# Kernel tuning notes

Hardware: AMD Instinct MI355X
Metric: run time of the kernel (lower is better)

Reference implementation:

```python
import jax, jax.numpy as jnp
import numpy as np

N = 100000
E = 1600000
IN_CH = 128
EDGE_CH = 16
HID = 128
OUT = 4
EPS = 1e-12  # F.normalize eps


def l2_normalize(x):
    # matches torch.nn.functional.normalize(x, p=2, dim=1)
    norm = jnp.sqrt(jnp.sum(x * x, axis=1, keepdims=True))
    return x / jnp.maximum(norm, EPS)


def sage_conv(x, row, col, edge_attr, W, b, n_nodes):
    # gather source node feats, concat edge feats: [E, in+edge]
    m = jnp.concatenate([x[row], edge_attr], axis=1)
    m = l2_normalize(m)
    # scatter-mean by destination node
    s = jax.ops.segment_sum(m, col, num_segments=n_nodes)
    cnt = jax.ops.segment_sum(jnp.ones((m.shape[0],), m.dtype), col, num_segments=n_nodes)
    agg = s / jnp.maximum(cnt, 1.0)[:, None]
    out = agg @ W + b
    return l2_normalize(out)


def setup_inputs() -> dict:
    key = jax.random.key(0)
    ks = jax.random.split(key, 7)
    x = jax.random.normal(ks[0], (N, IN_CH), dtype=jnp.float32)
    edge_index = jax.random.randint(ks[1], (2, E), 0, N, dtype=jnp.int64)
    edge_attr = jax.random.normal(ks[2], (E, EDGE_CH), dtype=jnp.float32)
    W1 = jax.random.normal(ks[3], (IN_CH + EDGE_CH, HID), dtype=jnp.float32) / np.sqrt(IN_CH + EDGE_CH)
    b1 = jnp.zeros((HID,), dtype=jnp.float32)
    W2 = jax.random.normal(ks[4], (HID + EDGE_CH, OUT), dtype=jnp.float32) / np.sqrt(HID + EDGE_CH)
    b2 = jnp.zeros((OUT,), dtype=jnp.float32)
    return {"x": x, "edge_index": edge_index, "edge_attr": edge_attr,
            "W1": W1, "b1": b1, "W2": W2, "b2": b2}


def reference(x, edge_index, edge_attr, W1, b1, W2, b2):
    row, col = edge_index[0], edge_index[1]
    h = sage_conv(x, row, col, edge_attr, W1, b1, N)
    h = jax.nn.relu(h)  # dropout is identity in eval mode
    h = sage_conv(h, row, col, edge_attr, W2, b2, N)
    return jax.nn.sigmoid(h)
```

## Files before the change

### kernel.cpp

```cpp
#include <hip/hip_runtime.h>
#include <hip/hip_fp16.h>
#include <math.h>

#define N_NODES 100000
#define N_EDGES 1600000
#define CHUNK 1024
#define NCHUNKS ((N_NODES + CHUNK - 1) / CHUNK)

union H8 { uint4 u; __half2 h[4]; };

__device__ __forceinline__ float red32(float v) {
    #pragma unroll
    for (int m = 16; m >= 1; m >>= 1) v += __shfl_xor(v, m, 64);
    return v;
}

__global__ __launch_bounds__(256) void hist(const int* __restrict__ col,
                                            int* __restrict__ cnt) {
    int e = blockIdx.x * blockDim.x + threadIdx.x;
    if (e >= N_EDGES) return;
    atomicAdd(&cnt[col[e]], 1);
}

__global__ void scan_part(const int* __restrict__ cnt, int* __restrict__ psum) {
    __shared__ int sd[CHUNK];
    int i = blockIdx.x * CHUNK + threadIdx.x;
    sd[threadIdx.x] = (i < N_NODES) ? cnt[i] : 0;
    __syncthreads();
    for (int s = CHUNK / 2; s > 0; s >>= 1) {
        if (threadIdx.x < s) sd[threadIdx.x] += sd[threadIdx.x + s];
        __syncthreads();
    }
    if (threadIdx.x == 0) psum[blockIdx.x] = sd[0];
}

__global__ void scan_top(const int* __restrict__ psum, int* __restrict__ coff,
                         int* __restrict__ off) {
    if (blockIdx.x == 0 && threadIdx.x == 0) {
        int run = 0;
        for (int i = 0; i < NCHUNKS; ++i) { coff[i] = run; run += psum[i]; }
        off[N_NODES] = N_EDGES;
    }
}

__global__ void scan_apply(const int* __restrict__ cnt, const int* __restrict__ coff,
                           int* __restrict__ off, int* __restrict__ head) {
    __shared__ int sd[CHUNK];
    int i = blockIdx.x * CHUNK + threadIdx.x;
    int v = (i < N_NODES) ? cnt[i] : 0;
    sd[threadIdx.x] = v;
    __syncthreads();
    for (int s = 1; s < CHUNK; s <<= 1) {
        int t = (threadIdx.x >= s) ? sd[threadIdx.x - s] : 0;
        __syncthreads();
        sd[threadIdx.x] += t;
        __syncthreads();
    }
    if (i < N_NODES) {
        int excl = coff[blockIdx.x] + sd[threadIdx.x] - v;
        off[i] = excl;
        head[i] = excl;
    }
}

__global__ __launch_bounds__(256) void gemm_y1h(const float* __restrict__ x,
                                                const float* __restrict__ W1,
                                                __half* __restrict__ y1h,
                                                float* __restrict__ nx) {
    __shared__ float xs[64][129];
    int r0 = blockIdx.x * 64;
    int t = threadIdx.x;
    for (int i = t; i < 64 * 32; i += 256) {
        int rr = i >> 5, c4 = (i & 31) * 4;
        int gr = r0 + rr;
        float4 v = (gr < N_NODES) ? *(const float4*)(x + (size_t)gr * 128 + c4)
                                  : make_float4(0.f, 0.f, 0.f, 0.f);
        xs[rr][c4] = v.x; xs[rr][c4 + 1] = v.y; xs[rr][c4 + 2] = v.z; xs[rr][c4 + 3] = v.w;
    }
    __syncthreads();
    {
        int rr = t >> 2, q = t & 3;
        float s = 0.f;
        #pragma unroll
        for (int k = 0; k < 32; ++k) { float v = xs[rr][q * 32 + k]; s += v * v; }
        s += __shfl_xor(s, 1, 64);
        s += __shfl_xor(s, 2, 64);
        if (q == 0 && r0 + rr < N_NODES) nx[r0 + rr] = s;
    }
    int tx = t & 31, ty = t >> 5;
    float4 acc[8];
    #pragma unroll
    for (int i = 0; i < 8; ++i) acc[i] = make_float4(0.f, 0.f, 0.f, 0.f);
    #pragma unroll 4
    for (int k = 0; k < 128; ++k) {
        float4 wv = *(const float4*)(W1 + (size_t)k * 128 + tx * 4);
        #pragma unroll
        for (int i = 0; i < 8; ++i) {
            float xv = xs[ty * 8 + i][k];
            acc[i].x += xv * wv.x; acc[i].y += xv * wv.y;
            acc[i].z += xv * wv.z; acc[i].w += xv * wv.w;
        }
    }
    #pragma unroll
    for (int i = 0; i < 8; ++i) {
        int rr = r0 + ty * 8 + i;
        if (rr < N_NODES) {
            H8 pk;
            pk.h[0] = __float22half2_rn(make_float2(acc[i].x, acc[i].y));
            pk.h[1] = __float22half2_rn(make_float2(acc[i].z, acc[i].w));
            *(uint2*)(y1h + (size_t)rr * 128 + tx * 4) = make_uint2(pk.u.x, pk.u.y);
        }
    }
}

__global__ __launch_bounds__(256) void scatter_e(
        const int* __restrict__ row, const int* __restrict__ col,
        const float* __restrict__ nx, const float* __restrict__ ea,
        int* __restrict__ head, int4* __restrict__ csrM) {
    int e = blockIdx.x * blockDim.x + threadIdx.x;
    if (e >= N_EDGES) return;
    const float4* p = (const float4*)(ea + (size_t)e * 16);
    float4 q0 = p[0], q1 = p[1], q2 = p[2], q3 = p[3];
    float s = q0.x*q0.x + q0.y*q0.y + q0.z*q0.z + q0.w*q0.w
            + q1.x*q1.x + q1.y*q1.y + q1.z*q1.z + q1.w*q1.w
            + q2.x*q2.x + q2.y*q2.y + q2.z*q2.z + q2.w*q2.w
            + q3.x*q3.x + q3.y*q3.y + q3.z*q3.z + q3.w*q3.w;
    int r = row[e];
    int c = col[e];
    float w1 = rsqrtf(fmaxf(nx[r] + s, 1e-24f));
    int pp = atomicAdd(&head[c], 1);
    int4 mt; mt.x = r; mt.y = __float_as_int(w1); mt.z = e; mt.w = __float_as_int(s);
    csrM[pp] = mt;
}

__global__ __launch_bounds__(256) void layer1(
        const __half* __restrict__ y1h, const float* __restrict__ ea,
        const int4* __restrict__ csrM, const int* __restrict__ off,
        const float* __restrict__ W1, const float* __restrict__ b1,
        const float* __restrict__ W2,
        float* __restrict__ hn, float4* __restrict__ peaC) {
    __shared__ int4  smeta[4][64];
    __shared__ float strans[4][144];
    int wv = threadIdx.x >> 6;
    int node = (blockIdx.x << 2) | wv;
    int lane = threadIdx.x & 63;
    if (node >= N_NODES) return;
    int s = off[node], e = off[node + 1];
    int deg = e - s;
    int m = (deg < 64) ? deg : 64;
    if (lane < m) smeta[wv][lane] = csrM[s + lane];
    asm volatile("s_waitcnt lgkmcnt(0)" ::: "memory");

    int e4 = lane >> 4;
    int c8 = lane & 15;
    int wrow = (c8 & 3) * 4;
    float4 w2r0 = *(const float4*)(W2 + (size_t)(128 + wrow + 0) * 4);
    float4 w2r1 = *(const float4*)(W2 + (size_t)(128 + wrow + 1) * 4);
    float4 w2r2 = *(const float4*)(W2 + (size_t)(128 + wrow + 2) * 4);
    float4 w2r3 = *(const float4*)(W2 + (size_t)(128 + wrow + 3) * 4);

    float4 a0 = make_float4(0,0,0,0), a1 = a0;
    float4 sea = a0;

    for (int t = 0; t < m; t += 4) {
        int idx = t + e4;
        bool val = idx < m;
        int4 mt = smeta[wv][val ? idx : 0];
        int r = mt.x;
        float w = val ? __int_as_float(mt.y) : 0.f;
        H8 pk; pk.u = *(const uint4*)(y1h + (size_t)r * 128 + c8 * 8);
        float2 f0 = __half22float2(pk.h[0]);
        float2 f1 = __half22float2(pk.h[1]);
        float2 f2 = __half22float2(pk.h[2]);
        float2 f3 = __half22float2(pk.h[3]);
        a0.x += f0.x * w; a0.y += f0.y * w; a0.z += f1.x * w; a0.w += f1.y * w;
        a1.x += f2.x * w; a1.y += f2.y * w; a1.z += f3.x * w; a1.w += f3.y * w;
        if (c8 < 4) {
            float4 ev = *(const float4*)(ea + (size_t)mt.z * 16 + c8 * 4);
            sea.x += ev.x * w; sea.y += ev.y * w;
            sea.z += ev.z * w; sea.w += ev.w * w;
            float4 pv;
            pv.x = ev.x*w2r0.x + ev.y*w2r1.x + ev.z*w2r2.x + ev.w*w2r3.x;
            pv.y = ev.x*w2r0.y + ev.y*w2r1.y + ev.z*w2r2.y + ev.w*w2r3.y;
            pv.z = ev.x*w2r0.z + ev.y*w2r1.z + ev.z*w2r2.z + ev.w*w2r3.z;
            pv.w = ev.x*w2r0.w + ev.y*w2r1.w + ev.z*w2r2.w + ev.w*w2r3.w;
            pv.x += __shfl_xor(pv.x, 1, 64); pv.y += __shfl_xor(pv.y, 1, 64);
            pv.z += __shfl_xor(pv.z, 1, 64); pv.w += __shfl_xor(pv.w, 1, 64);
            pv.x += __shfl_xor(pv.x, 2, 64); pv.y += __shfl_xor(pv.y, 2, 64);
            pv.z += __shfl_xor(pv.z, 2, 64); pv.w += __shfl_xor(pv.w, 2, 64);
            if (c8 == 0 && val) peaC[s + idx] = pv;
        }
    }
    for (int t = 64 + e4; t < deg; t += 4) {
        int4 mt = csrM[s + t];
        int r = mt.x;
        float w = __int_as_float(mt.y);
        H8 pk; pk.u = *(const uint4*)(y1h + (size_t)r * 128 + c8 * 8);
        float2 f0 = __half22float2(pk.h[0]);
        float2 f1 = __half22float2(pk.h[1]);
        float2 f2 = __half22float2(pk.h[2]);
        float2 f3 = __half22float2(pk.h[3]);
        a0.x += f0.x * w; a0.y += f0.y * w; a0.z += f1.x * w; a0.w += f1.y * w;
        a1.x += f2.x * w; a1.y += f2.y * w; a1.z += f3.x * w; a1.w += f3.y * w;
        if (c8 < 4) {
            float4 ev = *(const float4*)(ea + (size_t)mt.z * 16 + c8 * 4);
            sea.x += ev.x * w; sea.y += ev.y * w;
            sea.z += ev.z * w; sea.w += ev.w * w;
            float4 pv;
            pv.x = ev.x*w2r0.x + ev.y*w2r1.x + ev.z*w2r2.x + ev.w*w2r3.x;
            pv.y = ev.x*w2r0.y + ev.y*w2r1.y + ev.z*w2r2.y + ev.w*w2r3.y;
            pv.z = ev.x*w2r0.z + ev.y*w2r1.z + ev.z*w2r2.z + ev.w*w2r3.z;
            pv.w = ev.x*w2r0.w + ev.y*w2r1.w + ev.z*w2r2.w + ev.w*w2r3.w;
            pv.x += __shfl_xor(pv.x, 1, 64); pv.y += __shfl_xor(pv.y, 1, 64);
            pv.z += __shfl_xor(pv.z, 1, 64); pv.w += __shfl_xor(pv.w, 1, 64);
            pv.x += __shfl_xor(pv.x, 2, 64); pv.y += __shfl_xor(pv.y, 2, 64);
            pv.z += __shfl_xor(pv.z, 2, 64); pv.w += __shfl_xor(pv.w, 2, 64);
            if (c8 == 0) peaC[s + t] = pv;
        }
    }
    #pragma unroll
    for (int mm = 16; mm <= 32; mm <<= 1) {
        a0.x += __shfl_xor(a0.x, mm, 64); a0.y += __shfl_xor(a0.y, mm, 64);
        a0.z += __shfl_xor(a0.z, mm, 64); a0.w += __shfl_xor(a0.w, mm, 64);
        a1.x += __shfl_xor(a1.x, mm, 64); a1.y += __shfl_xor(a1.y, mm, 64);
        a1.z += __shfl_xor(a1.z, mm, 64); a1.w += __shfl_xor(a1.w, mm, 64);
        sea.x += __shfl_xor(sea.x, mm, 64); sea.y += __shfl_xor(sea.y, mm, 64);
        sea.z += __shfl_xor(sea.z, mm, 64); sea.w += __shfl_xor(sea.w, mm, 64);
    }
    if (e4 == 0) {
        *(float4*)&strans[wv][c8 * 8]     = a0;
        *(float4*)&strans[wv][c8 * 8 + 4] = a1;
        if (c8 < 4) *(float4*)&strans[wv][128 + c8 * 4] = sea;
    }
    asm volatile("s_waitcnt lgkmcnt(0)" ::: "memory");

    int c = lane & 31;
    float ic = 1.0f / fmaxf((float)deg, 1.0f);
    float4 av = *(const float4*)&strans[wv][c * 4];
    float4 b1v = *(const float4*)(b1 + c * 4);
    float4 o;
    o.x = av.x * ic + b1v.x; o.y = av.y * ic + b1v.y;
    o.z = av.z * ic + b1v.z; o.w = av.w * ic + b1v.w;
    #pragma unroll
    for (int k = 0; k < 16; ++k) {
        float sk = strans[wv][128 + k] * ic;
        float4 wv4 = *((const float4*)(W1 + (size_t)(128 + k) * 128) + c);
        o.x += sk * wv4.x; o.y += sk * wv4.y; o.z += sk * wv4.z; o.w += sk * wv4.w;
    }
    float ss    = o.x*o.x + o.y*o.y + o.z*o.z + o.w*o.w;
    float sspos = (o.x > 0.f ? o.x*o.x : 0.f) + (o.y > 0.f ? o.y*o.y : 0.f)
                + (o.z > 0.f ? o.z*o.z : 0.f) + (o.w > 0.f ? o.w*o.w : 0.f);
    ss = red32(ss);
    sspos = red32(sspos);
    float inv = rsqrtf(fmaxf(ss, 1e-24f));
    float4 h4;
    h4.x = fmaxf(o.x * inv, 0.f); h4.y = fmaxf(o.y * inv, 0.f);
    h4.z = fmaxf(o.z * inv, 0.f); h4.w = fmaxf(o.w * inv, 0.f);
    float nhv = sspos * inv * inv;
    float4 w0 = *(const float4*)(W2 + (size_t)(4*c + 0) * 4);
    float4 w1 = *(const float4*)(W2 + (size_t)(4*c + 1) * 4);
    float4 w2 = *(const float4*)(W2 + (size_t)(4*c + 2) * 4);
    float4 w3 = *(const float4*)(W2 + (size_t)(4*c + 3) * 4);
    float4 p;
    p.x = h4.x*w0.x + h4.y*w1.x + h4.z*w2.x + h4.w*w3.x;
    p.y = h4.x*w0.y + h4.y*w1.y + h4.z*w2.y + h4.w*w3.y;
    p.z = h4.x*w0.z + h4.y*w1.z + h4.z*w2.z + h4.w*w3.z;
    p.w = h4.x*w0.w + h4.y*w1.w + h4.z*w2.w + h4.w*w3.w;
    p.x = red32(p.x); p.y = red32(p.y); p.z = red32(p.z); p.w = red32(p.w);
    if (lane == 0) {
        *(float4*)(hn + (size_t)node * 8) = p;
        hn[(size_t)node * 8 + 4] = nhv;
    }
}

__global__ __launch_bounds__(256) void layer2(
        const int4* __restrict__ csrM, const float4* __restrict__ peaC,
        const float* __restrict__ hn, const int* __restrict__ off,
        const float* __restrict__ b2, float* __restrict__ out) {
    int wv = threadIdx.x >> 6;
    int node = (blockIdx.x << 2) | wv;
    int lane = threadIdx.x & 63;
    if (node >= N_NODES) return;
    int s = off[node], e = off[node + 1];
    int deg = e - s;
    float4 acc = make_float4(0.f, 0.f, 0.f, 0.f);
    for (int t = lane; t < deg; t += 64) {
        int4 mt = csrM[s + t];
        int r = mt.x;
        float sq = __int_as_float(mt.w);
        float4 yh = *(const float4*)(hn + (size_t)r * 8);
        float nh = hn[(size_t)r * 8 + 4];
        float w = rsqrtf(fmaxf(nh + sq, 1e-24f));
        float4 pe = peaC[s + t];
        acc.x += (yh.x + pe.x) * w; acc.y += (yh.y + pe.y) * w;
        acc.z += (yh.z + pe.z) * w; acc.w += (yh.w + pe.w) * w;
    }
    #pragma unroll
    for (int mm = 32; mm >= 1; mm >>= 1) {
        acc.x += __shfl_xor(acc.x, mm, 64);
        acc.y += __shfl_xor(acc.y, mm, 64);
        acc.z += __shfl_xor(acc.z, mm, 64);
        acc.w += __shfl_xor(acc.w, mm, 64);
    }
    if (lane == 0) {
        float ic = 1.0f / fmaxf((float)deg, 1.0f);
        float4 o;
        o.x = acc.x * ic + b2[0]; o.y = acc.y * ic + b2[1];
        o.z = acc.z * ic + b2[2]; o.w = acc.w * ic + b2[3];
        float ss = o.x*o.x + o.y*o.y + o.z*o.z + o.w*o.w;
        float inv = rsqrtf(fmaxf(ss, 1e-24f));
        float4 res;
        res.x = 1.0f / (1.0f + expf(-(o.x * inv)));
        res.y = 1.0f / (1.0f + expf(-(o.y * inv)));
        res.z = 1.0f / (1.0f + expf(-(o.z * inv)));
        res.w = 1.0f / (1.0f + expf(-(o.w * inv)));
        *(float4*)(out + (size_t)node * 4) = res;
    }
}

extern "C" void kernel_launch(void* const* d_in, const int* in_sizes, int n_in,
                              void* d_out, int out_size, void* d_ws, size_t ws_size,
                              hipStream_t stream) {
    const float* x   = (const float*)d_in[0];
    const int*   ei  = (const int*)d_in[1];
    const float* ea  = (const float*)d_in[2];
    const float* W1  = (const float*)d_in[3];
    const float* b1  = (const float*)d_in[4];
    const float* W2  = (const float*)d_in[5];
    const float* b2  = (const float*)d_in[6];
    const int* row = ei;
    const int* col = ei + N_EDGES;
    float* out = (float*)d_out;

    char* ws = (char*)d_ws;
    size_t o = 0;
    auto carve = [&](size_t bytes) { char* p = ws + o; o = (o + bytes + 255) & ~(size_t)255; return p; };
    __half* y1h    = (__half*)carve((size_t)N_NODES * 128 * 2);
    int4*   csrM   = (int4*)carve((size_t)N_EDGES * 16);
    float4* peaC   = (float4*)carve((size_t)N_EDGES * 16);
    int*    cnt    = (int*)carve((size_t)N_NODES * 4);
    int*    off    = (int*)carve((size_t)(N_NODES + 1) * 4);
    int*    head   = (int*)carve((size_t)N_NODES * 4);
    float*  nx     = (float*)carve((size_t)N_NODES * 4);
    float*  hn     = (float*)carve((size_t)N_NODES * 8 * 4);
    int*    psum   = (int*)carve((size_t)NCHUNKS * 4);
    int*    coff   = (int*)carve((size_t)NCHUNKS * 4);
    (void)ws_size; (void)in_sizes; (void)n_in; (void)out_size;

    hipMemsetAsync(cnt, 0, (size_t)N_NODES * 4, stream);

    dim3 b256(256);
    hist<<<(N_EDGES + 255) / 256, b256, 0, stream>>>(col, cnt);
    gemm_y1h<<<(N_NODES + 63) / 64, b256, 0, stream>>>(x, W1, y1h, nx);

    scan_part<<<NCHUNKS, CHUNK, 0, stream>>>(cnt, psum);
    scan_top<<<1, 64, 0, stream>>>(psum, coff, off);
    scan_apply<<<NCHUNKS, CHUNK, 0, stream>>>(cnt, coff, off, head);
    scatter_e<<<(N_EDGES + 255) / 256, b256, 0, stream>>>(row, col, nx, ea, head, csrM);

    layer1<<<(N_NODES + 3) / 4, b256, 0, stream>>>(y1h, ea, csrM, off, W1, b1, W2,
                                                   hn, peaC);
    layer2<<<(N_NODES + 3) / 4, b256, 0, stream>>>(csrM, peaC, hn, off, b2, out);
}
```

Baseline: 408.6 us.

## Drop per-edge projected edge-attr buffer; aggregate edge attrs in layer2 then project

Layer1 no longer computes and stores a per-edge projection of edge attributes through W2 (peaC, 25.6 MB written and read back). Layer2 instead re-reads the raw edge attributes, accumulates them weighted per node, and projects the aggregate once through W2. This also restructures layer2 to cache edge metadata in shared memory and use 16 edges x 4 lanes per wave. It trades a write plus read of peaC for a 64-byte gather of edge_attr per edge in layer2, and adds an unroll hint to layer1's main loop.

```diff
diff --git a/kernel.cpp b/kernel.cpp
--- a/kernel.cpp
+++ b/kernel.cpp
@@ -137,8 +137,7 @@
         const __half* __restrict__ y1h, const float* __restrict__ ea,
         const int4* __restrict__ csrM, const int* __restrict__ off,
         const float* __restrict__ W1, const float* __restrict__ b1,
-        const float* __restrict__ W2,
-        float* __restrict__ hn, float4* __restrict__ peaC) {
+        const float* __restrict__ W2, float* __restrict__ hn) {
     __shared__ int4  smeta[4][64];
     __shared__ float strans[4][144];
     int wv = threadIdx.x >> 6;
@@ -153,15 +152,10 @@
 
     int e4 = lane >> 4;
     int c8 = lane & 15;
-    int wrow = (c8 & 3) * 4;
-    float4 w2r0 = *(const float4*)(W2 + (size_t)(128 + wrow + 0) * 4);
-    float4 w2r1 = *(const float4*)(W2 + (size_t)(128 + wrow + 1) * 4);
-    float4 w2r2 = *(const float4*)(W2 + (size_t)(128 + wrow + 2) * 4);
-    float4 w2r3 = *(const float4*)(W2 + (size_t)(128 + wrow + 3) * 4);
-
     float4 a0 = make_float4(0,0,0,0), a1 = a0;
     float4 sea = a0;
 
+    #pragma unroll 2
     for (int t = 0; t < m; t += 4) {
         int idx = t + e4;
         bool val = idx < m;
@@ -179,16 +173,6 @@
             float4 ev = *(const float4*)(ea + (size_t)mt.z * 16 + c8 * 4);
             sea.x += ev.x * w; sea.y += ev.y * w;
             sea.z += ev.z * w; sea.w += ev.w * w;
-            float4 pv;
-            pv.x = ev.x*w2r0.x + ev.y*w2r1.x + ev.z*w2r2.x + ev.w*w2r3.x;
-            pv.y = ev.x*w2r0.y + ev.y*w2r1.y + ev.z*w2r2.y + ev.w*w2r3.y;
-            pv.z = ev.x*w2r0.z + ev.y*w2r1.z + ev.z*w2r2.z + ev.w*w2r3.z;
-            pv.w = ev.x*w2r0.w + ev.y*w2r1.w + ev.z*w2r2.w + ev.w*w2r3.w;
-            pv.x += __shfl_xor(pv.x, 1, 64); pv.y += __shfl_xor(pv.y, 1, 64);
-            pv.z += __shfl_xor(pv.z, 1, 64); pv.w += __shfl_xor(pv.w, 1, 64);
-            pv.x += __shfl_xor(pv.x, 2, 64); pv.y += __shfl_xor(pv.y, 2, 64);
-            pv.z += __shfl_xor(pv.z, 2, 64); pv.w += __shfl_xor(pv.w, 2, 64);
-            if (c8 == 0 && val) peaC[s + idx] = pv;
         }
     }
     for (int t = 64 + e4; t < deg; t += 4) {
@@ -206,16 +190,6 @@
             float4 ev = *(const float4*)(ea + (size_t)mt.z * 16 + c8 * 4);
             sea.x += ev.x * w; sea.y += ev.y * w;
             sea.z += ev.z * w; sea.w += ev.w * w;
-            float4 pv;
-            pv.x = ev.x*w2r0.x + ev.y*w2r1.x + ev.z*w2r2.x + ev.w*w2r3.x;
-            pv.y = ev.x*w2r0.y + ev.y*w2r1.y + ev.z*w2r2.y + ev.w*w2r3.y;
-            pv.z = ev.x*w2r0.z + ev.y*w2r1.z + ev.z*w2r2.z + ev.w*w2r3.z;
-            pv.w = ev.x*w2r0.w + ev.y*w2r1.w + ev.z*w2r2.w + ev.w*w2r3.w;
-            pv.x += __shfl_xor(pv.x, 1, 64); pv.y += __shfl_xor(pv.y, 1, 64);
-            pv.z += __shfl_xor(pv.z, 1, 64); pv.w += __shfl_xor(pv.w, 1, 64);
-            pv.x += __shfl_xor(pv.x, 2, 64); pv.y += __shfl_xor(pv.y, 2, 64);
-            pv.z += __shfl_xor(pv.z, 2, 64); pv.w += __shfl_xor(pv.w, 2, 64);
-            if (c8 == 0) peaC[s + t] = pv;
         }
     }
     #pragma unroll
@@ -274,39 +248,74 @@
 }
 
 __global__ __launch_bounds__(256) void layer2(
-        const int4* __restrict__ csrM, const float4* __restrict__ peaC,
+        const int4* __restrict__ csrM, const float* __restrict__ ea,
         const float* __restrict__ hn, const int* __restrict__ off,
-        const float* __restrict__ b2, float* __restrict__ out) {
+        const float* __restrict__ W2, const float* __restrict__ b2,
+        float* __restrict__ out) {
+    __shared__ int4 smeta[4][64];
     int wv = threadIdx.x >> 6;
     int node = (blockIdx.x << 2) | wv;
     int lane = threadIdx.x & 63;
     if (node >= N_NODES) return;
     int s = off[node], e = off[node + 1];
     int deg = e - s;
+    int m = (deg < 64) ? deg : 64;
+    if (lane < m) smeta[wv][lane] = csrM[s + lane];
+    asm volatile("s_waitcnt lgkmcnt(0)" ::: "memory");
+    int e16 = lane >> 2, q = lane & 3;
+    float4 w2r0 = *(const float4*)(W2 + (size_t)(128 + q * 4 + 0) * 4);
+    float4 w2r1 = *(const float4*)(W2 + (size_t)(128 + q * 4 + 1) * 4);
+    float4 w2r2 = *(const float4*)(W2 + (size_t)(128 + q * 4 + 2) * 4);
+    float4 w2r3 = *(const float4*)(W2 + (size_t)(128 + q * 4 + 3) * 4);
+
     float4 acc = make_float4(0.f, 0.f, 0.f, 0.f);
-    for (int t = lane; t < deg; t += 64) {
+    float4 sea = make_float4(0.f, 0.f, 0.f, 0.f);
+    for (int t = e16; t < m; t += 16) {
+        int4 mt = smeta[wv][t];
+        int r = mt.x;
+        float sq = __int_as_float(mt.w);
+        float nh = hn[(size_t)r * 8 + 4];
+        float w = rsqrtf(fmaxf(nh + sq, 1e-24f));
+        float4 yh = *(const float4*)(hn + (size_t)r * 8);
+        float4 ev = *(const float4*)(ea + (size_t)mt.z * 16 + q * 4);
+        acc.x += w * yh.x; acc.y += w * yh.y; acc.z += w * yh.z; acc.w += w * yh.w;
+        sea.x += w * ev.x; sea.y += w * ev.y; sea.z += w * ev.z; sea.w += w * ev.w;
+    }
+    for (int t = 64 + e16; t < deg; t += 16) {
         int4 mt = csrM[s + t];
         int r = mt.x;
         float sq = __int_as_float(mt.w);
-        float4 yh = *(const float4*)(hn + (size_t)r * 8);
         float nh = hn[(size_t)r * 8 + 4];
         float w = rsqrtf(fmaxf(nh + sq, 1e-24f));
-        float4 pe = peaC[s + t];
-        acc.x += (yh.x + pe.x) * w; acc.y += (yh.y + pe.y) * w;
-        acc.z += (yh.z + pe.z) * w; acc.w += (yh.w + pe.w) * w;
-    }
-    #pragma unroll
-    for (int mm = 32; mm >= 1; mm >>= 1) {
-        acc.x += __shfl_xor(acc.x, mm, 64);
-        acc.y += __shfl_xor(acc.y, mm, 64);
-        acc.z += __shfl_xor(acc.z, mm, 64);
-        acc.w += __shfl_xor(acc.w, mm, 64);
+        float4 yh = *(const float4*)(hn + (size_t)r * 8);
+        float4 ev = *(const float4*)(ea + (size_t)mt.z * 16 + q * 4);
+        acc.x += w * yh.x; acc.y += w * yh.y; acc.z += w * yh.z; acc.w += w * yh.w;
+        sea.x += w * ev.x; sea.y += w * ev.y; sea.z += w * ev.z; sea.w += w * ev.w;
+    }
+    #pragma unroll
+    for (int mm = 4; mm <= 32; mm <<= 1) {
+        acc.x += __shfl_xor(acc.x, mm, 64); acc.y += __shfl_xor(acc.y, mm, 64);
+        acc.z += __shfl_xor(acc.z, mm, 64); acc.w += __shfl_xor(acc.w, mm, 64);
+        sea.x += __shfl_xor(sea.x, mm, 64); sea.y += __shfl_xor(sea.y, mm, 64);
+        sea.z += __shfl_xor(sea.z, mm, 64); sea.w += __shfl_xor(sea.w, mm, 64);
+    }
+    float4 pv;
+    pv.x = sea.x*w2r0.x + sea.y*w2r1.x + sea.z*w2r2.x + sea.w*w2r3.x;
+    pv.y = sea.x*w2r0.y + sea.y*w2r1.y + sea.z*w2r2.y + sea.w*w2r3.y;
+    pv.z = sea.x*w2r0.z + sea.y*w2r1.z + sea.z*w2r2.z + sea.w*w2r3.z;
+    pv.w = sea.x*w2r0.w + sea.y*w2r1.w + sea.z*w2r2.w + sea.w*w2r3.w;
+    #pragma unroll
+    for (int mm = 1; mm <= 2; mm <<= 1) {
+        pv.x += __shfl_xor(pv.x, mm, 64); pv.y += __shfl_xor(pv.y, mm, 64);
+        pv.z += __shfl_xor(pv.z, mm, 64); pv.w += __shfl_xor(pv.w, mm, 64);
     }
     if (lane == 0) {
         float ic = 1.0f / fmaxf((float)deg, 1.0f);
         float4 o;
-        o.x = acc.x * ic + b2[0]; o.y = acc.y * ic + b2[1];
-        o.z = acc.z * ic + b2[2]; o.w = acc.w * ic + b2[3];
+        o.x = (acc.x + pv.x) * ic + b2[0];
+        o.y = (acc.y + pv.y) * ic + b2[1];
+        o.z = (acc.z + pv.z) * ic + b2[2];
+        o.w = (acc.w + pv.w) * ic + b2[3];
         float ss = o.x*o.x + o.y*o.y + o.z*o.z + o.w*o.w;
         float inv = rsqrtf(fmaxf(ss, 1e-24f));
         float4 res;
@@ -337,7 +346,6 @@
     auto carve = [&](size_t bytes) { char* p = ws + o; o = (o + bytes + 255) & ~(size_t)255; return p; };
     __half* y1h    = (__half*)carve((size_t)N_NODES * 128 * 2);
     int4*   csrM   = (int4*)carve((size_t)N_EDGES * 16);
-    float4* peaC   = (float4*)carve((size_t)N_EDGES * 16);
     int*    cnt    = (int*)carve((size_t)N_NODES * 4);
     int*    off    = (int*)carve((size_t)(N_NODES + 1) * 4);
     int*    head   = (int*)carve((size_t)N_NODES * 4);
@@ -358,7 +366,6 @@
     scan_apply<<<NCHUNKS, CHUNK, 0, stream>>>(cnt, coff, off, head);
     scatter_e<<<(N_EDGES + 255) / 256, b256, 0, stream>>>(row, col, nx, ea, head, csrM);
 
-    layer1<<<(N_NODES + 3) / 4, b256, 0, stream>>>(y1h, ea, csrM, off, W1, b1, W2,
-                                                   hn, peaC);
-    layer2<<<(N_NODES + 3) / 4, b256, 0, stream>>>(csrM, peaC, hn, off, b2, out);
-}
+    layer1<<<(N_NODES + 3) / 4, b256, 0, stream>>>(y1h, ea, csrM, off, W1, b1, W2, hn);
+    layer2<<<(N_NODES + 3) / 4, b256, 0, stream>>>(csrM, ea, hn, off, W2, b2, out);
+}
```

Result: faster. 386.1 us, median of 2 (-5.5%).

## Move layer-2 edge term into coalesced edge-order pass scattering to CSR slots

Applied to the files above, without the earlier changes.

Layer1 no longer computes or stores the per-edge edge_attr·W2 projection. A new edge-parallel pass reads edge_attr and row in original order, computes the squared norm, the W2 projection and the normalization weight, and writes the weighted contribution into the CSR slot recorded by scatter_e in a new epos array. The finish kernel then only sums the contiguous contributions per node. This makes the edge_attr reads coalesced and removes the random-access work from the layer-2 gather, at the cost of a scattered write, an extra epos array and one more launch. It also adds unroll 2 to the layer1 loop.

```diff
diff --git a/kernel.cpp b/kernel.cpp
--- a/kernel.cpp
+++ b/kernel.cpp
@@ -116,7 +116,7 @@
 __global__ __launch_bounds__(256) void scatter_e(
         const int* __restrict__ row, const int* __restrict__ col,
         const float* __restrict__ nx, const float* __restrict__ ea,
-        int* __restrict__ head, int4* __restrict__ csrM) {
+        int* __restrict__ head, int4* __restrict__ csrM, int* __restrict__ epos) {
     int e = blockIdx.x * blockDim.x + threadIdx.x;
     if (e >= N_EDGES) return;
     const float4* p = (const float4*)(ea + (size_t)e * 16);
@@ -131,14 +131,14 @@
     int pp = atomicAdd(&head[c], 1);
     int4 mt; mt.x = r; mt.y = __float_as_int(w1); mt.z = e; mt.w = __float_as_int(s);
     csrM[pp] = mt;
+    epos[e] = pp;
 }
 
 __global__ __launch_bounds__(256) void layer1(
         const __half* __restrict__ y1h, const float* __restrict__ ea,
         const int4* __restrict__ csrM, const int* __restrict__ off,
         const float* __restrict__ W1, const float* __restrict__ b1,
-        const float* __restrict__ W2,
-        float* __restrict__ hn, float4* __restrict__ peaC) {
+        const float* __restrict__ W2, float* __restrict__ hn) {
     __shared__ int4  smeta[4][64];
     __shared__ float strans[4][144];
     int wv = threadIdx.x >> 6;
@@ -153,15 +153,10 @@
 
     int e4 = lane >> 4;
     int c8 = lane & 15;
-    int wrow = (c8 & 3) * 4;
-    float4 w2r0 = *(const float4*)(W2 + (size_t)(128 + wrow + 0) * 4);
-    float4 w2r1 = *(const float4*)(W2 + (size_t)(128 + wrow + 1) * 4);
-    float4 w2r2 = *(const float4*)(W2 + (size_t)(128 + wrow + 2) * 4);
-    float4 w2r3 = *(const float4*)(W2 + (size_t)(128 + wrow + 3) * 4);
-
     float4 a0 = make_float4(0,0,0,0), a1 = a0;
     float4 sea = a0;
 
+    #pragma unroll 2
     for (int t = 0; t < m; t += 4) {
         int idx = t + e4;
         bool val = idx < m;
@@ -179,16 +174,6 @@
             float4 ev = *(const float4*)(ea + (size_t)mt.z * 16 + c8 * 4);
             sea.x += ev.x * w; sea.y += ev.y * w;
             sea.z += ev.z * w; sea.w += ev.w * w;
-            float4 pv;
-            pv.x = ev.x*w2r0.x + ev.y*w2r1.x + ev.z*w2r2.x + ev.w*w2r3.x;
-            pv.y = ev.x*w2r0.y + ev.y*w2r1.y + ev.z*w2r2.y + ev.w*w2r3.y;
-            pv.z = ev.x*w2r0.z + ev.y*w2r1.z + ev.z*w2r2.z + ev.w*w2r3.z;
-            pv.w = ev.x*w2r0.w + ev.y*w2r1.w + ev.z*w2r2.w + ev.w*w2r3.w;
-            pv.x += __shfl_xor(pv.x, 1, 64); pv.y += __shfl_xor(pv.y, 1, 64);
-            pv.z += __shfl_xor(pv.z, 1, 64); pv.w += __shfl_xor(pv.w, 1, 64);
-            pv.x += __shfl_xor(pv.x, 2, 64); pv.y += __shfl_xor(pv.y, 2, 64);
-            pv.z += __shfl_xor(pv.z, 2, 64); pv.w += __shfl_xor(pv.w, 2, 64);
-            if (c8 == 0 && val) peaC[s + idx] = pv;
         }
     }
     for (int t = 64 + e4; t < deg; t += 4) {
@@ -206,16 +191,6 @@
             float4 ev = *(const float4*)(ea + (size_t)mt.z * 16 + c8 * 4);
             sea.x += ev.x * w; sea.y += ev.y * w;
             sea.z += ev.z * w; sea.w += ev.w * w;
-            float4 pv;
-            pv.x = ev.x*w2r0.x + ev.y*w2r1.x + ev.z*w2r2.x + ev.w*w2r3.x;
-            pv.y = ev.x*w2r0.y + ev.y*w2r1.y + ev.z*w2r2.y + ev.w*w2r3.y;
-            pv.z = ev.x*w2r0.z + ev.y*w2r1.z + ev.z*w2r2.z + ev.w*w2r3.z;
-            pv.w = ev.x*w2r0.w + ev.y*w2r1.w + ev.z*w2r2.w + ev.w*w2r3.w;
-            pv.x += __shfl_xor(pv.x, 1, 64); pv.y += __shfl_xor(pv.y, 1, 64);
-            pv.z += __shfl_xor(pv.z, 1, 64); pv.w += __shfl_xor(pv.w, 1, 64);
-            pv.x += __shfl_xor(pv.x, 2, 64); pv.y += __shfl_xor(pv.y, 2, 64);
-            pv.z += __shfl_xor(pv.z, 2, 64); pv.w += __shfl_xor(pv.w, 2, 64);
-            if (c8 == 0) peaC[s + t] = pv;
         }
     }
     #pragma unroll
@@ -273,9 +248,42 @@
     }
 }
 
-__global__ __launch_bounds__(256) void layer2(
-        const int4* __restrict__ csrM, const float4* __restrict__ peaC,
-        const float* __restrict__ hn, const int* __restrict__ off,
+__global__ __launch_bounds__(256) void cpass(
+        const int* __restrict__ row, const float* __restrict__ ea,
+        const int* __restrict__ epos, const float* __restrict__ hn,
+        const float* __restrict__ W2, float4* __restrict__ cbuf) {
+    __shared__ float w2e[64];
+    int t = threadIdx.x;
+    if (t < 64) w2e[t] = W2[128 * 4 + t];
+    __syncthreads();
+    int e = blockIdx.x * 256 + t;
+    if (e >= N_EDGES) return;
+    const float4* p = (const float4*)(ea + (size_t)e * 16);
+    float4 q0 = p[0], q1 = p[1], q2 = p[2], q3 = p[3];
+    float a[16] = {q0.x,q0.y,q0.z,q0.w, q1.x,q1.y,q1.z,q1.w,
+                   q2.x,q2.y,q2.z,q2.w, q3.x,q3.y,q3.z,q3.w};
+    float s = 0.f;
+    float4 pv = make_float4(0.f, 0.f, 0.f, 0.f);
+    #pragma unroll
+    for (int k = 0; k < 16; ++k) {
+        s += a[k] * a[k];
+        pv.x += a[k] * w2e[k * 4 + 0];
+        pv.y += a[k] * w2e[k * 4 + 1];
+        pv.z += a[k] * w2e[k * 4 + 2];
+        pv.w += a[k] * w2e[k * 4 + 3];
+    }
+    int r = row[e];
+    float4 yh = *(const float4*)(hn + (size_t)r * 8);
+    float nh = hn[(size_t)r * 8 + 4];
+    float w = rsqrtf(fmaxf(nh + s, 1e-24f));
+    float4 cv;
+    cv.x = (yh.x + pv.x) * w; cv.y = (yh.y + pv.y) * w;
+    cv.z = (yh.z + pv.z) * w; cv.w = (yh.w + pv.w) * w;
+    cbuf[epos[e]] = cv;
+}
+
+__global__ __launch_bounds__(256) void finish(
+        const float4* __restrict__ cbuf, const int* __restrict__ off,
         const float* __restrict__ b2, float* __restrict__ out) {
     int wv = threadIdx.x >> 6;
     int node = (blockIdx.x << 2) | wv;
@@ -285,15 +293,8 @@
     int deg = e - s;
     float4 acc = make_float4(0.f, 0.f, 0.f, 0.f);
     for (int t = lane; t < deg; t += 64) {
-        int4 mt = csrM[s + t];
-        int r = mt.x;
-        float sq = __int_as_float(mt.w);
-        float4 yh = *(const float4*)(hn + (size_t)r * 8);
-        float nh = hn[(size_t)r * 8 + 4];
-        float w = rsqrtf(fmaxf(nh + sq, 1e-24f));
-        float4 pe = peaC[s + t];
-        acc.x += (yh.x + pe.x) * w; acc.y += (yh.y + pe.y) * w;
-        acc.z += (yh.z + pe.z) * w; acc.w += (yh.w + pe.w) * w;
+        float4 cv = cbuf[s + t];
+        acc.x += cv.x; acc.y += cv.y; acc.z += cv.z; acc.w += cv.w;
     }
     #pragma unroll
     for (int mm = 32; mm >= 1; mm >>= 1) {
@@ -337,7 +338,8 @@
     auto carve = [&](size_t bytes) { char* p = ws + o; o = (o + bytes + 255) & ~(size_t)255; return p; };
     __half* y1h    = (__half*)carve((size_t)N_NODES * 128 * 2);
     int4*   csrM   = (int4*)carve((size_t)N_EDGES * 16);
-    float4* peaC   = (float4*)carve((size_t)N_EDGES * 16);
+    int*    epos   = (int*)carve((size_t)N_EDGES * 4);
+    float4* cbuf   = (float4*)carve((size_t)N_EDGES * 16);
     int*    cnt    = (int*)carve((size_t)N_NODES * 4);
     int*    off    = (int*)carve((size_t)(N_NODES + 1) * 4);
     int*    head   = (int*)carve((size_t)N_NODES * 4);
@@ -356,9 +358,10 @@
     scan_part<<<NCHUNKS, CHUNK, 0, stream>>>(cnt, psum);
     scan_top<<<1, 64, 0, stream>>>(psum, coff, off);
     scan_apply<<<NCHUNKS, CHUNK, 0, stream>>>(cnt, coff, off, head);
-    scatter_e<<<(N_EDGES + 255) / 256, b256, 0, stream>>>(row, col, nx, ea, head, csrM);
-
-    layer1<<<(N_NODES + 3) / 4, b256, 0, stream>>>(y1h, ea, csrM, off, W1, b1, W2,
-                                                   hn, peaC);
-    layer2<<<(N_NODES + 3) / 4, b256, 0, stream>>>(csrM, peaC, hn, off, b2, out);
-}
+    scatter_e<<<(N_EDGES + 255) / 256, b256, 0, stream>>>(row, col, nx, ea, head,
+                                                          csrM, epos);
+
+    layer1<<<(N_NODES + 3) / 4, b256, 0, stream>>>(y1h, ea, csrM, off, W1, b1, W2, hn);
+    cpass<<<(N_EDGES + 255) / 256, b256, 0, stream>>>(row, ea, epos, hn, W2, cbuf);
+    finish<<<(N_NODES + 3) / 4, b256, 0, stream>>>(cbuf, off, b2, out);
+}
```

Result: slower. 419.4 us (+2.6%).
